# Optimization experiments

Hardware: AMD Instinct MI355X
Metric: run time of the kernel (lower is better)

The kernel has to match this reference:

```python
import jax, jax.numpy as jnp
import numpy as np

B, D, S = 4096, 1024, 1024

def setup_inputs() -> dict:
    key = jax.random.key(0)
    ks = jax.random.split(key, 12)
    u = lambda k, shp: jax.random.uniform(k, shp, jnp.float32, -0.05, 0.05)
    return {
        "inputs": jax.random.normal(ks[0], (B, D), jnp.float32),
        "h0": jax.random.normal(ks[1], (B, S), jnp.float32),
        "c0": jax.random.normal(ks[2], (B, S), jnp.float32),
        "w_f": u(ks[3], (D, S)), "u_f": u(ks[4], (S, S)), "b_f": u(ks[5], (S,)),
        "w_i": u(ks[6], (D, S)), "u_i": u(ks[7], (S, S)), "b_i": u(ks[8], (S,)),
        "w_o": u(ks[9], (D, S)), "u_o": u(ks[10], (S, S)), "b_o": u(ks[11], (S,)),
    }

def reference(inputs, h0, c0, w_f, u_f, b_f, w_i, u_i, b_i, w_o, u_o, b_o):
    # Faithful to the original: input_cell reuses the FORGET gate weights and
    # sigmoid (not tanh, not w_c) -- a quirk of the source module.
    pre_f = inputs @ w_f + h0 @ u_f + b_f          # [B, S]
    forget_gate = jax.nn.sigmoid(pre_f)
    input_gate = jax.nn.sigmoid(inputs @ w_i + h0 @ u_i + b_i)
    output_gate = jax.nn.sigmoid(inputs @ w_o + h0 @ u_o + b_o)
    input_cell = jax.nn.sigmoid(pre_f)             # same pre-activation as forget gate
    c_new = forget_gate * c0 + input_cell * input_gate
    h_new = output_gate * jnp.tanh(c_new)
    return (h_new, c_new)
```

## Files before the change

kernel.cpp:

```cpp
#include <hip/hip_runtime.h>
#include <cstdint>
#include <cstddef>


typedef __attribute__((ext_vector_type(8))) short bf16x8;
typedef __attribute__((ext_vector_type(4))) float f32x4;
typedef __attribute__((ext_vector_type(8))) short s16x8;
typedef __attribute__((ext_vector_type(4))) float f32x4v;

#define MROWS 4096
#define KDIM  1024
#define NCOLS 1024

__device__ __forceinline__ short f2bf(float f) {
    uint32_t u = __builtin_bit_cast(uint32_t, f);
    u += 0x7fffu + ((u >> 16) & 1u);
    return (short)(u >> 16);
}

__global__ void cvt_bf16_kernel(const float* __restrict__ x,
                                const float* __restrict__ h,
                                short* __restrict__ xb,
                                short* __restrict__ hb) {
    int b = blockIdx.x;
    const float* in;
    short* out;
    if (b < 2048) { in = x; out = xb; }
    else          { in = h; out = hb; b -= 2048; }
    const int i = (b * 256 + threadIdx.x) * 8;
    f32x4v a = *(const f32x4v*)(in + i);
    f32x4v c = *(const f32x4v*)(in + i + 4);
    s16x8 o;
    o[0] = f2bf(a[0]); o[1] = f2bf(a[1]); o[2] = f2bf(a[2]); o[3] = f2bf(a[3]);
    o[4] = f2bf(c[0]); o[5] = f2bf(c[1]); o[6] = f2bf(c[2]); o[7] = f2bf(c[3]);
    *(s16x8*)(out + i) = o;
}

struct W6 {
    const float* src[6];
    short* dst[6];
};

__global__ void transpose_cvt_kernel(W6 p) {
    __shared__ short tile[32][33];
    const float* __restrict__ w  = p.src[blockIdx.z];
    short* __restrict__       wt = p.dst[blockIdx.z];
    const int tx = threadIdx.x & 31;
    const int ty = threadIdx.x >> 5;
    const int kbase = blockIdx.y * 32;
    const int nbase = blockIdx.x * 32;
#pragma unroll
    for (int r = 0; r < 4; ++r) {
        int k = kbase + ty + r * 8;
        tile[ty + r * 8][tx] = f2bf(w[k * NCOLS + nbase + tx]);
    }
    __syncthreads();
#pragma unroll
    for (int r = 0; r < 4; ++r) {
        int n = nbase + ty + r * 8;
        wt[n * KDIM + kbase + tx] = tile[tx][ty + r * 8];
    }
}

__global__ __launch_bounds__(512, 2)
void lstm_gemm_kernel(const short* __restrict__ Xb, const short* __restrict__ Hb,
                      const short* __restrict__ WT0, const short* __restrict__ WT1,
                      const short* __restrict__ WT2,
                      const short* __restrict__ UT0, const short* __restrict__ UT1,
                      const short* __restrict__ UT2,
                      const float* __restrict__ bf_, const float* __restrict__ bi_,
                      const float* __restrict__ bo_,
                      const float* __restrict__ c0,
                      float* __restrict__ outH, float* __restrict__ outC) {
    __shared__ __align__(16) short lds[4][16384];

    const int tid  = threadIdx.x;
    const int lane = tid & 63;
    const int wave = tid >> 6;
    const int wm   = wave >> 2;
    const int wn   = wave & 3;
    const int m0   = blockIdx.y * 128;
    const int n0   = blockIdx.x * 128;

    const int l15 = lane & 15;
    const int q   = lane >> 4;

    f32x4 acc[3][4][2] = {};

    const int srow   = tid >> 2;
    const int schunk = (tid & 3) ^ ((tid >> 3) & 3);
    const int skoff  = schunk * 8;

    int aOff[4], bOff[2];
#pragma unroll
    for (int m = 0; m < 4; ++m) {
        const int row = wm * 64 + m * 16 + l15;
        aOff[m] = row * 64 + ((q ^ ((row >> 1) & 3)) << 4);
    }
#pragma unroll
    for (int n = 0; n < 2; ++n) {
        const int row = wn * 32 + n * 16 + l15;
        bOff[n] = row * 64 + ((q ^ ((row >> 1) & 3)) << 4);
    }

    auto stage = [&](int buf, int kt) {
        const bool second = kt >= 32;
        const short* aS = second ? Hb  : Xb;
        const short* s0 = second ? UT0 : WT0;
        const short* s1 = second ? UT1 : WT1;
        const short* s2 = second ? UT2 : WT2;
        const int kk = (kt & 31) * 32 + skoff;
#pragma unroll
        for (int r = 0; r < 4; ++r) {
            const short* src = (r == 0) ? aS : (r == 1 ? s0 : (r == 2 ? s1 : s2));
            const int rbase = (r == 0) ? m0 : n0;
            const char* g = (const char*)(src + (size_t)(rbase + srow) * KDIM + kk);
            __builtin_amdgcn_global_load_lds(
                (const __attribute__((address_space(1))) unsigned int*)(uintptr_t)g,
                (__attribute__((address_space(3))) unsigned int*)(uintptr_t)
                    ((char*)&lds[buf][0] + r * 8192 + tid * 16),
                16, 0, 0);
        }
    };

    bf16x8 fa0[4], fb0[6], fa1[4], fb1[6];

#define READF(FA, FB, BUF)                                                   \
    {                                                                        \
        const char* L_ = (const char*)&lds[(BUF)][0];                        \
        _Pragma("unroll")                                                    \
        for (int m_ = 0; m_ < 4; ++m_)                                       \
            FA[m_] = *(const bf16x8*)(L_ + aOff[m_]);                        \
        _Pragma("unroll")                                                    \
        for (int g_ = 0; g_ < 3; ++g_)                                       \
            _Pragma("unroll")                                                \
            for (int n_ = 0; n_ < 2; ++n_)                                   \
                FB[g_ * 2 + n_] =                                            \
                    *(const bf16x8*)(L_ + 8192 * (1 + g_) + bOff[n_]);       \
    }

#define MFMAC(FA, FB)                                                        \
    {                                                                        \
        __builtin_amdgcn_s_setprio(1);                                       \
        _Pragma("unroll")                                                    \
        for (int g_ = 0; g_ < 3; ++g_)                                       \
            _Pragma("unroll")                                                \
            for (int n_ = 0; n_ < 2; ++n_)                                   \
                _Pragma("unroll")                                            \
                for (int m_ = 0; m_ < 4; ++m_)                               \
                    acc[g_][m_][n_] = __builtin_amdgcn_mfma_f32_16x16x32_bf16(\
                        FA[m_], FB[g_ * 2 + n_], acc[g_][m_][n_], 0, 0, 0);  \
        __builtin_amdgcn_s_setprio(0);                                       \
    }

#define WAITV(N) asm volatile("s_waitcnt vmcnt(" #N ")" ::: "memory")
#define WAITL0   asm volatile("s_waitcnt lgkmcnt(0)" ::: "memory")
#define BAR      __builtin_amdgcn_s_barrier()
#define SCHED0   __builtin_amdgcn_sched_barrier(0)

    stage(0, 0);
    stage(1, 1);
    stage(2, 2);
    WAITV(8);
    BAR;
    SCHED0;
    READF(fa0, fb0, 0);
    WAITL0;

    for (int kt = 0; kt < 60; kt += 2) {
        stage((kt + 3) & 3, kt + 3);
        WAITV(8);
        BAR;
        SCHED0;
        READF(fa1, fb1, (kt + 1) & 3);
        SCHED0;
        MFMAC(fa0, fb0);
        SCHED0;
        WAITL0;
        stage((kt + 4) & 3, kt + 4);
        WAITV(8);
        BAR;
        SCHED0;
        READF(fa0, fb0, (kt + 2) & 3);
        SCHED0;
        MFMAC(fa1, fb1);
        SCHED0;
        WAITL0;
    }

    stage(63 & 3, 63);
    WAITV(8);
    BAR;
    SCHED0;
    READF(fa1, fb1, 61 & 3);
    SCHED0;
    MFMAC(fa0, fb0);
    SCHED0;
    WAITL0;

    WAITV(4);
    BAR;
    SCHED0;
    READF(fa0, fb0, 62 & 3);
    SCHED0;
    MFMAC(fa1, fb1);
    SCHED0;
    WAITL0;

    WAITV(0);
    BAR;
    SCHED0;
    READF(fa1, fb1, 63 & 3);
    SCHED0;
    MFMAC(fa0, fb0);
    SCHED0;
    WAITL0;

    MFMAC(fa1, fb1);

    const int rj = (lane >> 4) * 4;
#pragma unroll
    for (int m = 0; m < 4; ++m) {
#pragma unroll
        for (int n = 0; n < 2; ++n) {
            const int col = n0 + wn * 32 + n * 16 + l15;
            const float bfv = bf_[col], biv = bi_[col], bov = bo_[col];
            const f32x4 pf = acc[0][m][n];
            const f32x4 pi = acc[1][m][n];
            const f32x4 po = acc[2][m][n];
#pragma unroll
            for (int j = 0; j < 4; ++j) {
                const int row = m0 + wm * 64 + m * 16 + rj + j;
                const float fg = 1.f / (1.f + __expf(-(pf[j] + bfv)));
                const float ig = 1.f / (1.f + __expf(-(pi[j] + biv)));
                const float og = 1.f / (1.f + __expf(-(po[j] + bov)));
                const float cv = c0[row * NCOLS + col];
                const float cn = fg * cv + fg * ig;
                const float e  = __expf(-2.f * cn);
                const float th = (1.f - e) / (1.f + e);
                outH[row * NCOLS + col] = og * th;
                outC[row * NCOLS + col] = cn;
            }
        }
    }
#undef READF
#undef MFMAC
#undef WAITV
#undef WAITL0
#undef BAR
#undef SCHED0
}

extern "C" void kernel_launch(void* const* d_in, const int* in_sizes, int n_in,
                              void* d_out, int out_size, void* d_ws, size_t ws_size,
                              hipStream_t stream) {
    const float* inputs = (const float*)d_in[0];
    const float* h0     = (const float*)d_in[1];
    const float* c0     = (const float*)d_in[2];
    const float* w_f    = (const float*)d_in[3];
    const float* u_f    = (const float*)d_in[4];
    const float* b_f    = (const float*)d_in[5];
    const float* w_i    = (const float*)d_in[6];
    const float* u_i    = (const float*)d_in[7];
    const float* b_i    = (const float*)d_in[8];
    const float* w_o    = (const float*)d_in[9];
    const float* u_o    = (const float*)d_in[10];
    const float* b_o    = (const float*)d_in[11];

    float* outH = (float*)d_out;
    float* outC = outH + (size_t)MROWS * NCOLS;

    char* ws = (char*)d_ws;
    short* Xb  = (short*)(ws);
    short* Hb  = (short*)(ws + (8u << 20));
    short* WT0 = (short*)(ws + (16u << 20));
    short* WT1 = (short*)(ws + (18u << 20));
    short* WT2 = (short*)(ws + (20u << 20));
    short* UT0 = (short*)(ws + (22u << 20));
    short* UT1 = (short*)(ws + (24u << 20));
    short* UT2 = (short*)(ws + (26u << 20));

    cvt_bf16_kernel<<<4096, 256, 0, stream>>>(inputs, h0, Xb, Hb);

    W6 p;
    p.src[0] = w_f; p.src[1] = w_i; p.src[2] = w_o;
    p.src[3] = u_f; p.src[4] = u_i; p.src[5] = u_o;
    p.dst[0] = WT0; p.dst[1] = WT1; p.dst[2] = WT2;
    p.dst[3] = UT0; p.dst[4] = UT1; p.dst[5] = UT2;
    transpose_cvt_kernel<<<dim3(32, 32, 6), 256, 0, stream>>>(p);

    dim3 grid(NCOLS / 128, MROWS / 128);
    lstm_gemm_kernel<<<grid, 512, 0, stream>>>(
        Xb, Hb, WT0, WT1, WT2, UT0, UT1, UT2,
        b_f, b_i, b_o, c0, outH, outC);
}
```

Baseline: 76.90 us.

## Pre-pack weights in MFMA fragment order and load B directly to registers

The weight transpose kernel now writes bf16 weights in a layout that matches each lane's MFMA B-fragment, so the GEMM loads B fragments straight from global memory into registers, bypassing LDS. Only the A tile still goes through LDS, which cuts LDS footprint from 128KB to 32KB per block and removes the B-side LDS writes and reads. The trade-off is that B loads now go to global/L2 with per-wave redundancy across the wm rows and add latency exposure, and the vmcnt wait counts had to be retuned.

```diff
diff --git a/kernel.cpp b/kernel.cpp
--- a/kernel.cpp
+++ b/kernel.cpp
@@ -44,7 +44,7 @@
 __global__ void transpose_cvt_kernel(W6 p) {
     __shared__ short tile[32][33];
     const float* __restrict__ w  = p.src[blockIdx.z];
-    short* __restrict__       wt = p.dst[blockIdx.z];
+    short* __restrict__       wp = p.dst[blockIdx.z];
     const int tx = threadIdx.x & 31;
     const int ty = threadIdx.x >> 5;
     const int kbase = blockIdx.y * 32;
@@ -52,27 +52,36 @@
 #pragma unroll
     for (int r = 0; r < 4; ++r) {
         int k = kbase + ty + r * 8;
-        tile[ty + r * 8][tx] = f2bf(w[k * NCOLS + nbase + tx]);
+        tile[ty + r * 8][nbase + tx - nbase] = f2bf(w[k * NCOLS + nbase + tx]);
     }
     __syncthreads();
-#pragma unroll
-    for (int r = 0; r < 4; ++r) {
-        int n = nbase + ty + r * 8;
-        wt[n * KDIM + kbase + tx] = tile[tx][ty + r * 8];
+    const int u = threadIdx.x;
+    if (u < 128) {
+        const int j8  = u & 3;
+        const int nl  = u >> 2;
+        s16x8 v;
+#pragma unroll
+        for (int jj = 0; jj < 8; ++jj)
+            v[jj] = tile[j8 * 8 + jj][nl];
+        const int n    = nbase + nl;
+        const int t    = n >> 4;
+        const int c    = blockIdx.y;
+        const int lane = j8 * 16 + (n & 15);
+        *(s16x8*)(wp + ((size_t)((t * 32 + c) * 64 + lane)) * 8) = v;
     }
 }
 
 __global__ __launch_bounds__(512, 2)
 void lstm_gemm_kernel(const short* __restrict__ Xb, const short* __restrict__ Hb,
-                      const short* __restrict__ WT0, const short* __restrict__ WT1,
-                      const short* __restrict__ WT2,
-                      const short* __restrict__ UT0, const short* __restrict__ UT1,
-                      const short* __restrict__ UT2,
+                      const short* __restrict__ WP0, const short* __restrict__ WP1,
+                      const short* __restrict__ WP2,
+                      const short* __restrict__ UP0, const short* __restrict__ UP1,
+                      const short* __restrict__ UP2,
                       const float* __restrict__ bf_, const float* __restrict__ bi_,
                       const float* __restrict__ bo_,
                       const float* __restrict__ c0,
                       float* __restrict__ outH, float* __restrict__ outC) {
-    __shared__ __align__(16) short lds[4][16384];
+    __shared__ __align__(16) short lds[4][4096];
 
     const int tid  = threadIdx.x;
     const int lane = tid & 63;
@@ -81,62 +90,62 @@
     const int wn   = wave & 3;
     const int m0   = blockIdx.y * 128;
     const int n0   = blockIdx.x * 128;
+    const int bx8  = blockIdx.x * 8;
 
     const int l15 = lane & 15;
     const int q   = lane >> 4;
 
     f32x4 acc[3][4][2] = {};
 
-    const int srow   = tid >> 2;
-    const int schunk = (tid & 3) ^ ((tid >> 3) & 3);
-    const int skoff  = schunk * 8;
-
-    int aOff[4], bOff[2];
+    const int srow  = tid >> 2;
+    const int skoff = ((tid & 3) ^ ((tid >> 3) & 3)) * 8;
+
+    int aOff[4];
 #pragma unroll
     for (int m = 0; m < 4; ++m) {
         const int row = wm * 64 + m * 16 + l15;
         aOff[m] = row * 64 + ((q ^ ((row >> 1) & 3)) << 4);
     }
-#pragma unroll
-    for (int n = 0; n < 2; ++n) {
-        const int row = wn * 32 + n * 16 + l15;
-        bOff[n] = row * 64 + ((q ^ ((row >> 1) & 3)) << 4);
-    }
-
-    auto stage = [&](int buf, int kt) {
-        const bool second = kt >= 32;
-        const short* aS = second ? Hb  : Xb;
-        const short* s0 = second ? UT0 : WT0;
-        const short* s1 = second ? UT1 : WT1;
-        const short* s2 = second ? UT2 : WT2;
-        const int kk = (kt & 31) * 32 + skoff;
-#pragma unroll
-        for (int r = 0; r < 4; ++r) {
-            const short* src = (r == 0) ? aS : (r == 1 ? s0 : (r == 2 ? s1 : s2));
-            const int rbase = (r == 0) ? m0 : n0;
-            const char* g = (const char*)(src + (size_t)(rbase + srow) * KDIM + kk);
-            __builtin_amdgcn_global_load_lds(
-                (const __attribute__((address_space(1))) unsigned int*)(uintptr_t)g,
-                (__attribute__((address_space(3))) unsigned int*)(uintptr_t)
-                    ((char*)&lds[buf][0] + r * 8192 + tid * 16),
-                16, 0, 0);
-        }
+
+    auto stageA = [&](int buf, int kt) {
+        const short* src = (kt >= 32) ? Hb : Xb;
+        const char* g = (const char*)(src + (size_t)(m0 + srow) * KDIM +
+                                      (kt & 31) * 32 + skoff);
+        __builtin_amdgcn_global_load_lds(
+            (const __attribute__((address_space(1))) unsigned int*)(uintptr_t)g,
+            (__attribute__((address_space(3))) unsigned int*)(uintptr_t)
+                ((char*)&lds[buf][0] + tid * 16),
+            16, 0, 0);
     };
 
-    bf16x8 fa0[4], fb0[6], fa1[4], fb1[6];
-
-#define READF(FA, FB, BUF)                                                   \
+    bf16x8 fa0[4], fa1[4], fb0[6], fb1[6];
+
+#define LOADB(FB, KT)                                                        \
     {                                                                        \
-        const char* L_ = (const char*)&lds[(BUF)][0];                        \
+        const int kt_ = (KT);                                                \
+        const bool sec_ = kt_ >= 32;                                         \
+        const short* b0_ = sec_ ? UP0 : WP0;                                 \
+        const short* b1_ = sec_ ? UP1 : WP1;                                 \
+        const short* b2_ = sec_ ? UP2 : WP2;                                 \
+        const int c_ = kt_ & 31;                                             \
         _Pragma("unroll")                                                    \
-        for (int m_ = 0; m_ < 4; ++m_)                                       \
-            FA[m_] = *(const bf16x8*)(L_ + aOff[m_]);                        \
-        _Pragma("unroll")                                                    \
-        for (int g_ = 0; g_ < 3; ++g_)                                       \
+        for (int g_ = 0; g_ < 3; ++g_) {                                     \
+            const short* base_ = (g_ == 0) ? b0_ : (g_ == 1 ? b1_ : b2_);    \
             _Pragma("unroll")                                                \
-            for (int n_ = 0; n_ < 2; ++n_)                                   \
-                FB[g_ * 2 + n_] =                                            \
-                    *(const bf16x8*)(L_ + 8192 * (1 + g_) + bOff[n_]);       \
+            for (int nf_ = 0; nf_ < 2; ++nf_) {                              \
+                const int t_ = bx8 + wn * 2 + nf_;                           \
+                FB[g_ * 2 + nf_] = *(const bf16x8*)(base_ +                  \
+                    ((size_t)((t_ * 32 + c_) * 64 + lane)) * 8);             \
+            }                                                                \
+        }                                                                    \
+    }
+
+#define READA(FA, BUF)                                                      \
+    {                                                                       \
+        const char* L_ = (const char*)&lds[(BUF)][0];                       \
+        _Pragma("unroll")                                                   \
+        for (int m_ = 0; m_ < 4; ++m_)                                      \
+            FA[m_] = *(const bf16x8*)(L_ + aOff[m_]);                       \
     }
 
 #define MFMAC(FA, FB)                                                        \
@@ -158,64 +167,74 @@
 #define BAR      __builtin_amdgcn_s_barrier()
 #define SCHED0   __builtin_amdgcn_sched_barrier(0)
 
-    stage(0, 0);
-    stage(1, 1);
-    stage(2, 2);
+    stageA(0, 0);
+    stageA(1, 1);
+    LOADB(fb0, 0);
+    stageA(2, 2);
     WAITV(8);
     BAR;
     SCHED0;
-    READF(fa0, fb0, 0);
+    READA(fa0, 0);
     WAITL0;
 
     for (int kt = 0; kt < 60; kt += 2) {
-        stage((kt + 3) & 3, kt + 3);
+        LOADB(fb1, kt + 1);
+        SCHED0;
+        stageA((kt + 3) & 3, kt + 3);
+        SCHED0;
         WAITV(8);
         BAR;
         SCHED0;
-        READF(fa1, fb1, (kt + 1) & 3);
+        READA(fa1, (kt + 1) & 3);
         SCHED0;
         MFMAC(fa0, fb0);
-        SCHED0;
         WAITL0;
-        stage((kt + 4) & 3, kt + 4);
+        LOADB(fb0, kt + 2);
+        SCHED0;
+        stageA((kt + 4) & 3, kt + 4);
+        SCHED0;
         WAITV(8);
         BAR;
         SCHED0;
-        READF(fa0, fb0, (kt + 2) & 3);
+        READA(fa0, (kt + 2) & 3);
         SCHED0;
         MFMAC(fa1, fb1);
-        SCHED0;
         WAITL0;
     }
 
-    stage(63 & 3, 63);
+    LOADB(fb1, 61);
+    SCHED0;
+    stageA(63 & 3, 63);
+    SCHED0;
     WAITV(8);
     BAR;
     SCHED0;
-    READF(fa1, fb1, 61 & 3);
+    READA(fa1, 61 & 3);
     SCHED0;
     MFMAC(fa0, fb0);
-    SCHED0;
     WAITL0;
 
-    WAITV(4);
+    LOADB(fb0, 62);
+    SCHED0;
+    WAITV(7);
     BAR;
     SCHED0;
-    READF(fa0, fb0, 62 & 3);
+    READA(fa0, 62 & 3);
     SCHED0;
     MFMAC(fa1, fb1);
-    SCHED0;
     WAITL0;
 
+    LOADB(fb1, 63);
+    SCHED0;
+    WAITV(6);
+    BAR;
+    SCHED0;
+    READA(fa1, 63 & 3);
+    SCHED0;
+    MFMAC(fa0, fb0);
+    WAITL0;
+
     WAITV(0);
-    BAR;
-    SCHED0;
-    READF(fa1, fb1, 63 & 3);
-    SCHED0;
-    MFMAC(fa0, fb0);
-    SCHED0;
-    WAITL0;
-
     MFMAC(fa1, fb1);
 
     const int rj = (lane >> 4) * 4;
@@ -243,7 +262,8 @@
             }
         }
     }
-#undef READF
+#undef LOADB
+#undef READA
 #undef MFMAC
 #undef WAITV
 #undef WAITL0
@@ -273,24 +293,24 @@
     char* ws = (char*)d_ws;
     short* Xb  = (short*)(ws);
     short* Hb  = (short*)(ws + (8u << 20));
-    short* WT0 = (short*)(ws + (16u << 20));
-    short* WT1 = (short*)(ws + (18u << 20));
-    short* WT2 = (short*)(ws + (20u << 20));
-    short* UT0 = (short*)(ws + (22u << 20));
-    short* UT1 = (short*)(ws + (24u << 20));
-    short* UT2 = (short*)(ws + (26u << 20));
+    short* WP0 = (short*)(ws + (16u << 20));
+    short* WP1 = (short*)(ws + (18u << 20));
+    short* WP2 = (short*)(ws + (20u << 20));
+    short* UP0 = (short*)(ws + (22u << 20));
+    short* UP1 = (short*)(ws + (24u << 20));
+    short* UP2 = (short*)(ws + (26u << 20));
 
     cvt_bf16_kernel<<<4096, 256, 0, stream>>>(inputs, h0, Xb, Hb);
 
     W6 p;
     p.src[0] = w_f; p.src[1] = w_i; p.src[2] = w_o;
     p.src[3] = u_f; p.src[4] = u_i; p.src[5] = u_o;
-    p.dst[0] = WT0; p.dst[1] = WT1; p.dst[2] = WT2;
-    p.dst[3] = UT0; p.dst[4] = UT1; p.dst[5] = UT2;
+    p.dst[0] = WP0; p.dst[1] = WP1; p.dst[2] = WP2;
+    p.dst[3] = UP0; p.dst[4] = UP1; p.dst[5] = UP2;
     transpose_cvt_kernel<<<dim3(32, 32, 6), 256, 0, stream>>>(p);
 
     dim3 grid(NCOLS / 128, MROWS / 128);
     lstm_gemm_kernel<<<grid, 512, 0, stream>>>(
-        Xb, Hb, WT0, WT1, WT2, UT0, UT1, UT2,
+        Xb, Hb, WP0, WP1, WP2, UP0, UP1, UP2,
         b_f, b_i, b_o, c0, outH, outC);
 }
```

Result: slower. 80.09 us (+4.1%).
